# Kernel tuning notes

Measured on AMD Instinct MI355X. Metric: run time of the kernel, lower is better.

The kernel has to match this reference:

```python
import math
import jax, jax.numpy as jnp
import numpy as np

N, CH3, T = 64, 192, 2048

def setup_inputs() -> dict:
    key = jax.random.key(0)
    qkv = jax.random.normal(key, (N, CH3, T), dtype=jnp.float32)
    return {"qkv": qkv}

def reference(qkv):
    ch = qkv.shape[1] // 3
    q, k, v = jnp.split(qkv, 3, axis=1)  # each [b, c, t]
    scale = 1.0 / math.sqrt(math.sqrt(ch))
    # [b, t, s] score matrix (faithful to the naive implementation)
    weight = jnp.einsum('bct,bcs->bts', q * scale, k * scale)
    weight = jax.nn.softmax(weight.astype(jnp.float32), axis=-1).astype(weight.dtype)
    return jnp.einsum('bts,bcs->bct', weight, v)
```

## Files before the change

kernel.cpp:

```cpp
#include <hip/hip_runtime.h>
#include <math.h>


#define B_   64
#define CH_  64
#define T_   2048
#define TQ   128
#define SB   64
#define NIT  (T_ / SB)

typedef __attribute__((ext_vector_type(8))) short short8;
typedef __attribute__((ext_vector_type(4))) float f32x4;
typedef __attribute__((ext_vector_type(4))) unsigned short us4;
typedef __attribute__((ext_vector_type(8))) unsigned short us8;

static __device__ __forceinline__ unsigned short f2bf(float f) {
    union { float f; unsigned u; } v; v.f = f;
    unsigned r = v.u + 0x7FFFu + ((v.u >> 16) & 1u);
    return (unsigned short)(r >> 16);
}

static __device__ __forceinline__ short8 ld_contig(const unsigned short* p) {
    return *(const short8*)p;
}

static __device__ __forceinline__ short8 ld_strided(const unsigned short* p, int stride) {
    short8 r;
#pragma unroll
    for (int j = 0; j < 8; ++j) r[j] = (short)p[j * stride];
    return r;
}

static __device__ __forceinline__ void gl_lds16(const unsigned short* g, unsigned short* l) {
    __builtin_amdgcn_global_load_lds(
        (const __attribute__((address_space(1))) unsigned int*)g,
        (__attribute__((address_space(3))) unsigned int*)l, 16, 0, 0);
}

static __device__ __forceinline__ float vexp2(float x) {
#if __has_builtin(__builtin_amdgcn_exp2f)
    return __builtin_amdgcn_exp2f(x);
#else
    float r;
    asm("v_exp_f32 %0, %1\n\ts_nop 1" : "=v"(r) : "v"(x));
    return r;
#endif
}

static __device__ __forceinline__ unsigned cvtpk(float lo, float hi) {
    unsigned r;
    asm("v_cvt_pk_bf16_f32 %0, %1, %2" : "=v"(r) : "v"(lo), "v"(hi));
    return r;
}

static __device__ __forceinline__ void pl_swap(unsigned& a, unsigned& b) {
    asm volatile("v_permlane32_swap_b32 %0, %1" : "+v"(a), "+v"(b));
    asm volatile("v_permlane16_swap_b32 %0, %1" : "+v"(a), "+v"(b));
}

__global__ __launch_bounds__(256) void qkv_prep(const float* __restrict__ qkv,
                                                unsigned short* __restrict__ Ktg,
                                                unsigned short* __restrict__ Vbg)
{
    __shared__ float Tl[64][65];
    const int tid = threadIdx.x;
    const int b   = blockIdx.x >> 5;
    const int t0  = (blockIdx.x & 31) * 64;
    const float* Kp = qkv + (size_t)b * (3 * CH_ * T_) + (size_t)CH_ * T_;
    const float* Vp = Kp + (size_t)CH_ * T_;

    {
        const int c = tid & 63, fq = tid >> 6;
#pragma unroll
        for (int k = 0; k < 4; ++k) {
            const int tl = 16 * fq + 4 * k;
            const float4 v = *(const float4*)(Kp + (size_t)c * T_ + t0 + tl);
            Tl[c][tl] = v.x; Tl[c][tl + 1] = v.y; Tl[c][tl + 2] = v.z; Tl[c][tl + 3] = v.w;
        }
    }
    {
        const int c = tid >> 2, tq = (tid & 3) * 16;
        unsigned short* vout = Vbg + (size_t)b * CH_ * T_ + (size_t)c * T_ + t0 + tq;
        const float* vin = Vp + (size_t)c * T_ + t0 + tq;
#pragma unroll
        for (int k = 0; k < 2; ++k) {
            const float4 a  = *(const float4*)(vin + 8 * k);
            const float4 bq = *(const float4*)(vin + 8 * k + 4);
            us8 w8;
            w8[0]=f2bf(a.x);  w8[1]=f2bf(a.y);  w8[2]=f2bf(a.z);  w8[3]=f2bf(a.w);
            w8[4]=f2bf(bq.x); w8[5]=f2bf(bq.y); w8[6]=f2bf(bq.z); w8[7]=f2bf(bq.w);
            *(us8*)(vout + 8 * k) = w8;
        }
    }
    __syncthreads();
    {
        const int cb = tid & 7;
#pragma unroll
        for (int ot = 0; ot < 2; ++ot) {
            const int sl = (tid >> 3) + 32 * ot;
            us8 w8;
#pragma unroll
            for (int j = 0; j < 8; ++j) w8[j] = f2bf(Tl[8 * cb + j][sl]);
            *(us8*)(Ktg + (size_t)b * T_ * CH_ + (size_t)(t0 + sl) * 64 + 8 * cb) = w8;
        }
    }
}

__global__ __launch_bounds__(256, 4) void qkv_attn5(const float* __restrict__ qkv,
                                                    const unsigned short* __restrict__ Ktg,
                                                    const unsigned short* __restrict__ Vbg,
                                                    float* __restrict__ out)
{
    __shared__ unsigned short Ks[2][64 * 64];
    __shared__ unsigned short Vs[2][64 * 64];

    const int tid  = threadIdx.x;
    const int lane = tid & 63;
    const int wid  = tid >> 6;
    const int l15  = lane & 15;
    const int h    = lane >> 4;

    int bid = blockIdx.x;
    bid = (bid & 7) * 128 + (bid >> 3);
    const int b  = bid >> 4;
    const int t0 = (bid & 15) * TQ;
    const int tb = t0 + wid * 32;

    const float* Qp = qkv + (size_t)b * (3 * CH_ * T_);
    const unsigned short* Ktb = Ktg + (size_t)b * (T_ * CH_);
    const unsigned short* Vbb = Vbg + (size_t)b * (CH_ * T_);

    const int x0 = 8 * ((h)     ^ (l15 & 7));
    const int x1 = 8 * ((4 + h) ^ (l15 & 7));
    const int rb = l15 * 64;

    const int r0 = tid >> 3;
    const int kx = (tid & 7) ^ (r0 & 7);
    const unsigned short* ksrc0 = Ktb + (size_t)r0 * 64 + 8 * kx;
    const unsigned short* vsrc0 = Vbb + (size_t)r0 * T_ + 8 * kx;

    short8 aq[2][2];
#pragma unroll
    for (int ts = 0; ts < 2; ++ts)
#pragma unroll
        for (int ch = 0; ch < 2; ++ch) {
            short8 q;
#pragma unroll
            for (int j = 0; j < 8; ++j)
                q[j] = (short)f2bf(0.180336880f *
                        Qp[(size_t)(32 * ch + 8 * h + j) * T_ + tb + 16 * ts + l15]);
            aq[ts][ch] = q;
        }

    f32x4 o[4][2];
#pragma unroll
    for (int cs = 0; cs < 4; ++cs)
#pragma unroll
        for (int ts = 0; ts < 2; ++ts) o[cs][ts] = (f32x4){0.f, 0.f, 0.f, 0.f};
    float dsum[2] = {0.f, 0.f};
    const f32x4 zero4 = {0.f, 0.f, 0.f, 0.f};

    gl_lds16(ksrc0,                   &Ks[0][wid * 512]);
    gl_lds16(ksrc0 + 32 * 64,         &Ks[0][wid * 512 + 2048]);
    gl_lds16(vsrc0,                   &Vs[0][wid * 512]);
    gl_lds16(vsrc0 + (size_t)32 * T_, &Vs[0][wid * 512 + 2048]);

    for (int it = 0; it < NIT; ++it) {
        __syncthreads();
        const int buf = it & 1;
        if (it + 1 < NIT) {
            const int s1 = (it + 1) * SB;
            const int bo = (buf ^ 1) * 4096;
            gl_lds16(ksrc0 + (size_t)s1 * 64,        &Ks[0][bo + wid * 512]);
            gl_lds16(ksrc0 + (size_t)(s1 + 32) * 64, &Ks[0][bo + wid * 512 + 2048]);
            gl_lds16(vsrc0 + s1,                     &Vs[0][bo + wid * 512]);
            gl_lds16(vsrc0 + (size_t)32 * T_ + s1,   &Vs[0][bo + wid * 512 + 2048]);
        }
        const unsigned short* kb = &Ks[buf][0];
        const unsigned short* vb = &Vs[buf][0];

        short8 pb[2][2];
#pragma unroll
        for (int half = 0; half < 2; ++half) {
            f32x4 w[2][2];
            __builtin_amdgcn_s_setprio(1);
#pragma unroll
            for (int ss2 = 0; ss2 < 2; ++ss2) {
                const int ss = 2 * half + ss2;
                const short8 bk0 = ld_contig(kb + rb + ss * 1024 + x0);
                const short8 bk1 = ld_contig(kb + rb + ss * 1024 + x1);
#pragma unroll
                for (int ts = 0; ts < 2; ++ts) {
                    f32x4 acc = zero4;
                    acc = __builtin_amdgcn_mfma_f32_16x16x32_bf16(bk0, aq[ts][0], acc, 0, 0, 0);
                    acc = __builtin_amdgcn_mfma_f32_16x16x32_bf16(bk1, aq[ts][1], acc, 0, 0, 0);
                    w[ts][ss2] = acc;
                }
            }
            __builtin_amdgcn_s_setprio(0);
#pragma unroll
            for (int ts = 0; ts < 2; ++ts) {
                float e0[4], e1[4];
#pragma unroll
                for (int r = 0; r < 4; ++r) {
                    e0[r] = vexp2(w[ts][0][r]);
                    e1[r] = vexp2(w[ts][1][r]);
                }
                dsum[ts] += ((e0[0] + e0[1]) + (e0[2] + e0[3]))
                          + ((e1[0] + e1[1]) + (e1[2] + e1[3]));
                unsigned a0 = cvtpk(e0[0], e0[1]);
                unsigned a1 = cvtpk(e0[2], e0[3]);
                unsigned b0 = cvtpk(e1[0], e1[1]);
                unsigned b1 = cvtpk(e1[2], e1[3]);
                pl_swap(a0, b0);
                pl_swap(a1, b1);
                union { short8 s8; unsigned u[4]; } u;
                u.u[0] = a0; u.u[1] = a1; u.u[2] = b0; u.u[3] = b1;
                pb[ts][half] = u.s8;
            }
        }

        __builtin_amdgcn_s_setprio(1);
#pragma unroll
        for (int cs = 0; cs < 4; ++cs) {
            const short8 av0 = ld_contig(vb + rb + cs * 1024 + x0);
            const short8 av1 = ld_contig(vb + rb + cs * 1024 + x1);
#pragma unroll
            for (int ts = 0; ts < 2; ++ts) {
                o[cs][ts] = __builtin_amdgcn_mfma_f32_16x16x32_bf16(av0, pb[ts][0], o[cs][ts], 0, 0, 0);
                o[cs][ts] = __builtin_amdgcn_mfma_f32_16x16x32_bf16(av1, pb[ts][1], o[cs][ts], 0, 0, 0);
            }
        }
        __builtin_amdgcn_s_setprio(0);
    }

    float inv[2];
#pragma unroll
    for (int ts = 0; ts < 2; ++ts) {
        float d = dsum[ts];
        d += __shfl_xor(d, 16, 64);
        d += __shfl_xor(d, 32, 64);
        inv[ts] = 1.0f / d;
    }

    float* outp = out + (size_t)b * CH_ * T_;
#pragma unroll
    for (int cs = 0; cs < 4; ++cs)
#pragma unroll
        for (int r = 0; r < 4; ++r) {
            const size_t row = (size_t)(16 * cs + 4 * h + r) * T_;
            outp[row + tb + l15]      = o[cs][0][r] * inv[0];
            outp[row + tb + 16 + l15] = o[cs][1][r] * inv[1];
        }
}

__global__ __launch_bounds__(256) void qkv_attn_fb(const float* __restrict__ qkv,
                                                   float* __restrict__ out)
{
    __shared__ unsigned short Qs[CH_][68];
    __shared__ unsigned short Ksf[CH_][68];
    __shared__ unsigned short Vsf[CH_][72];
    __shared__ unsigned short Psf[4][64][18];

    const int tid  = threadIdx.x;
    const int lane = tid & 63;
    const int wid  = tid >> 6;
    const int l15  = lane & 15;
    const int h    = lane >> 4;
    const int bidx = blockIdx.x;
    const int b    = bidx >> 5;
    const int t0   = (bidx & 31) * 64;
    const int tw   = wid * 16;

    const float* Qp = qkv + (size_t)b * (3 * CH_ * T_);
    const float* Kp = Qp + CH_ * T_;
    const float* Vp = Kp + CH_ * T_;

    const int srow = tid >> 4;
    const int scol = (tid & 15) << 2;

#pragma unroll
    for (int i = 0; i < 4; ++i) {
        const int c = srow + 16 * i;
        const float4 q = *(const float4*)(Qp + (size_t)c * T_ + t0 + scol);
        us4 w; w[0] = f2bf(q.x); w[1] = f2bf(q.y); w[2] = f2bf(q.z); w[3] = f2bf(q.w);
        *(us4*)(&Qs[c][scol]) = w;
    }
    __syncthreads();

    const short8 aq0 = ld_strided(&Qs[0 + 8 * h][tw + l15], 68);
    const short8 aq1 = ld_strided(&Qs[32 + 8 * h][tw + l15], 68);

    short8 aones;
#pragma unroll
    for (int j = 0; j < 8; ++j) aones[j] = (short)0x3F80;

    f32x4 o[4];
#pragma unroll
    for (int cs = 0; cs < 4; ++cs) o[cs] = (f32x4){0.f, 0.f, 0.f, 0.f};
    float l_run = 0.0f;
    const f32x4 zero4 = {0.f, 0.f, 0.f, 0.f};

    for (int it = 0; it < 32; ++it) {
        const int s0 = it * 64;
        __syncthreads();
#pragma unroll
        for (int i = 0; i < 4; ++i) {
            const int c = srow + 16 * i;
            const float4 kv = *(const float4*)(Kp + (size_t)c * T_ + s0 + scol);
            us4 wk; wk[0] = f2bf(kv.x); wk[1] = f2bf(kv.y); wk[2] = f2bf(kv.z); wk[3] = f2bf(kv.w);
            *(us4*)(&Ksf[c][scol]) = wk;
            const float4 vv = *(const float4*)(Vp + (size_t)c * T_ + s0 + scol);
            us4 wv; wv[0] = f2bf(vv.x); wv[1] = f2bf(vv.y); wv[2] = f2bf(vv.z); wv[3] = f2bf(vv.w);
            *(us4*)(&Vsf[c][scol]) = wv;
        }
        __syncthreads();

        f32x4 w[4];
#pragma unroll
        for (int ss = 0; ss < 4; ++ss) {
            const short8 bkl = ld_strided(&Ksf[0 + 8 * h][ss * 16 + l15], 68);
            const short8 bkh = ld_strided(&Ksf[32 + 8 * h][ss * 16 + l15], 68);
            f32x4 acc = zero4;
            acc = __builtin_amdgcn_mfma_f32_16x16x32_bf16(aq0, bkl, acc, 0, 0, 0);
            acc = __builtin_amdgcn_mfma_f32_16x16x32_bf16(aq1, bkh, acc, 0, 0, 0);
            w[ss] = acc;
        }

#pragma unroll
        for (int ss = 0; ss < 4; ++ss) {
            const float e0 = __expf(0.125f * w[ss][0]);
            const float e1 = __expf(0.125f * w[ss][1]);
            const float e2 = __expf(0.125f * w[ss][2]);
            const float e3 = __expf(0.125f * w[ss][3]);
            const unsigned p01 = (unsigned)f2bf(e0) | ((unsigned)f2bf(e1) << 16);
            const unsigned p23 = (unsigned)f2bf(e2) | ((unsigned)f2bf(e3) << 16);
            const int s = ss * 16 + l15;
            *(unsigned*)(&Psf[wid][s][4 * h]) = p01;
            *(unsigned*)(&Psf[wid][s][4 * h + 2]) = p23;
        }

        const short8 pb0 = ld_strided(&Psf[wid][0 + 8 * h][l15], 18);
        const short8 pb1 = ld_strided(&Psf[wid][32 + 8 * h][l15], 18);

        f32x4 lacc = zero4;
        lacc = __builtin_amdgcn_mfma_f32_16x16x32_bf16(aones, pb0, lacc, 0, 0, 0);
        lacc = __builtin_amdgcn_mfma_f32_16x16x32_bf16(aones, pb1, lacc, 0, 0, 0);
        l_run += lacc[0];

#pragma unroll
        for (int cs = 0; cs < 4; ++cs) {
            const short8 av0 = ld_contig(&Vsf[cs * 16 + l15][0 + 8 * h]);
            const short8 av1 = ld_contig(&Vsf[cs * 16 + l15][32 + 8 * h]);
            o[cs] = __builtin_amdgcn_mfma_f32_16x16x32_bf16(av0, pb0, o[cs], 0, 0, 0);
            o[cs] = __builtin_amdgcn_mfma_f32_16x16x32_bf16(av1, pb1, o[cs], 0, 0, 0);
        }
    }

    const float invd = 1.0f / l_run;
    float* outp = out + (size_t)b * CH_ * T_;
#pragma unroll
    for (int cs = 0; cs < 4; ++cs)
#pragma unroll
        for (int r = 0; r < 4; ++r)
            outp[(size_t)(cs * 16 + 4 * h + r) * T_ + t0 + tw + l15] = o[cs][r] * invd;
}

extern "C" void kernel_launch(void* const* d_in, const int* in_sizes, int n_in,
                              void* d_out, int out_size, void* d_ws, size_t ws_size,
                              hipStream_t stream) {
    const float* qkv = (const float*)d_in[0];
    float* outp = (float*)d_out;
    const size_t need = (size_t)2 * B_ * CH_ * T_ * sizeof(unsigned short);
    if (ws_size >= need) {
        unsigned short* Ktg = (unsigned short*)d_ws;
        unsigned short* Vbg = Ktg + (size_t)B_ * T_ * CH_;
        qkv_prep<<<dim3(B_ * 32), dim3(256), 0, stream>>>(qkv, Ktg, Vbg);
        qkv_attn5<<<dim3(B_ * (T_ / TQ)), dim3(256), 0, stream>>>(qkv, Ktg, Vbg, outp);
    } else {
        qkv_attn_fb<<<dim3(B_ * 32), dim3(256), 0, stream>>>(qkv, outp);
    }
}
```

Measured before the change: 98.10 us.

## Use two waves per block with 64 query columns per wave

After: 101.5 us. 1.03x slower.

```diff
diff --git a/kernel.cpp b/kernel.cpp
--- a/kernel.cpp
+++ b/kernel.cpp
@@ -106,7 +106,7 @@
     }
 }
 
-__global__ __launch_bounds__(256, 4) void qkv_attn5(const float* __restrict__ qkv,
+__global__ __launch_bounds__(128, 2) void qkv_attn6(const float* __restrict__ qkv,
                                                     const unsigned short* __restrict__ Ktg,
                                                     const unsigned short* __restrict__ Vbg,
                                                     float* __restrict__ out)
@@ -124,7 +124,7 @@
     bid = (bid & 7) * 128 + (bid >> 3);
     const int b  = bid >> 4;
     const int t0 = (bid & 15) * TQ;
-    const int tb = t0 + wid * 32;
+    const int tb = t0 + wid * 64;
 
     const float* Qp = qkv + (size_t)b * (3 * CH_ * T_);
     const unsigned short* Ktb = Ktg + (size_t)b * (T_ * CH_);
@@ -138,10 +138,11 @@
     const int kx = (tid & 7) ^ (r0 & 7);
     const unsigned short* ksrc0 = Ktb + (size_t)r0 * 64 + 8 * kx;
     const unsigned short* vsrc0 = Vbb + (size_t)r0 * T_ + 8 * kx;
-
-    short8 aq[2][2];
-#pragma unroll
-    for (int ts = 0; ts < 2; ++ts)
+    const int dbase = 8 * wid * 64;
+
+    short8 aq[4][2];
+#pragma unroll
+    for (int ts = 0; ts < 4; ++ts)
 #pragma unroll
         for (int ch = 0; ch < 2; ++ch) {
             short8 q;
@@ -152,18 +153,19 @@
             aq[ts][ch] = q;
         }
 
-    f32x4 o[4][2];
+    f32x4 o[4][4];
 #pragma unroll
     for (int cs = 0; cs < 4; ++cs)
 #pragma unroll
-        for (int ts = 0; ts < 2; ++ts) o[cs][ts] = (f32x4){0.f, 0.f, 0.f, 0.f};
-    float dsum[2] = {0.f, 0.f};
+        for (int ts = 0; ts < 4; ++ts) o[cs][ts] = (f32x4){0.f, 0.f, 0.f, 0.f};
+    float dsum[4] = {0.f, 0.f, 0.f, 0.f};
     const f32x4 zero4 = {0.f, 0.f, 0.f, 0.f};
 
-    gl_lds16(ksrc0,                   &Ks[0][wid * 512]);
-    gl_lds16(ksrc0 + 32 * 64,         &Ks[0][wid * 512 + 2048]);
-    gl_lds16(vsrc0,                   &Vs[0][wid * 512]);
-    gl_lds16(vsrc0 + (size_t)32 * T_, &Vs[0][wid * 512 + 2048]);
+#pragma unroll
+    for (int j = 0; j < 4; ++j) {
+        gl_lds16(ksrc0 + (size_t)(16 * j) * 64,  &Ks[0][16 * j * 64 + dbase]);
+        gl_lds16(vsrc0 + (size_t)(16 * j) * T_,  &Vs[0][16 * j * 64 + dbase]);
+    }
 
     for (int it = 0; it < NIT; ++it) {
         __syncthreads();
@@ -171,18 +173,21 @@
         if (it + 1 < NIT) {
             const int s1 = (it + 1) * SB;
             const int bo = (buf ^ 1) * 4096;
-            gl_lds16(ksrc0 + (size_t)s1 * 64,        &Ks[0][bo + wid * 512]);
-            gl_lds16(ksrc0 + (size_t)(s1 + 32) * 64, &Ks[0][bo + wid * 512 + 2048]);
-            gl_lds16(vsrc0 + s1,                     &Vs[0][bo + wid * 512]);
-            gl_lds16(vsrc0 + (size_t)32 * T_ + s1,   &Vs[0][bo + wid * 512 + 2048]);
+#pragma unroll
+            for (int j = 0; j < 4; ++j) {
+                gl_lds16(ksrc0 + (size_t)(s1 + 16 * j) * 64,
+                         &Ks[0][bo + 16 * j * 64 + dbase]);
+                gl_lds16(vsrc0 + (size_t)(16 * j) * T_ + s1,
+                         &Vs[0][bo + 16 * j * 64 + dbase]);
+            }
         }
         const unsigned short* kb = &Ks[buf][0];
         const unsigned short* vb = &Vs[buf][0];
 
-        short8 pb[2][2];
+        short8 pb[4][2];
 #pragma unroll
         for (int half = 0; half < 2; ++half) {
-            f32x4 w[2][2];
+            f32x4 w[4][2];
             __builtin_amdgcn_s_setprio(1);
 #pragma unroll
             for (int ss2 = 0; ss2 < 2; ++ss2) {
@@ -190,7 +195,7 @@
                 const short8 bk0 = ld_contig(kb + rb + ss * 1024 + x0);
                 const short8 bk1 = ld_contig(kb + rb + ss * 1024 + x1);
 #pragma unroll
-                for (int ts = 0; ts < 2; ++ts) {
+                for (int ts = 0; ts < 4; ++ts) {
                     f32x4 acc = zero4;
                     acc = __builtin_amdgcn_mfma_f32_16x16x32_bf16(bk0, aq[ts][0], acc, 0, 0, 0);
                     acc = __builtin_amdgcn_mfma_f32_16x16x32_bf16(bk1, aq[ts][1], acc, 0, 0, 0);
@@ -199,7 +204,7 @@
             }
             __builtin_amdgcn_s_setprio(0);
 #pragma unroll
-            for (int ts = 0; ts < 2; ++ts) {
+            for (int ts = 0; ts < 4; ++ts) {
                 float e0[4], e1[4];
 #pragma unroll
                 for (int r = 0; r < 4; ++r) {
@@ -226,7 +231,7 @@
             const short8 av0 = ld_contig(vb + rb + cs * 1024 + x0);
             const short8 av1 = ld_contig(vb + rb + cs * 1024 + x1);
 #pragma unroll
-            for (int ts = 0; ts < 2; ++ts) {
+            for (int ts = 0; ts < 4; ++ts) {
                 o[cs][ts] = __builtin_amdgcn_mfma_f32_16x16x32_bf16(av0, pb[ts][0], o[cs][ts], 0, 0, 0);
                 o[cs][ts] = __builtin_amdgcn_mfma_f32_16x16x32_bf16(av1, pb[ts][1], o[cs][ts], 0, 0, 0);
             }
@@ -234,9 +239,9 @@
         __builtin_amdgcn_s_setprio(0);
     }
 
-    float inv[2];
-#pragma unroll
-    for (int ts = 0; ts < 2; ++ts) {
+    float inv[4];
+#pragma unroll
+    for (int ts = 0; ts < 4; ++ts) {
         float d = dsum[ts];
         d += __shfl_xor(d, 16, 64);
         d += __shfl_xor(d, 32, 64);
@@ -249,8 +254,9 @@
 #pragma unroll
         for (int r = 0; r < 4; ++r) {
             const size_t row = (size_t)(16 * cs + 4 * h + r) * T_;
-            outp[row + tb + l15]      = o[cs][0][r] * inv[0];
-            outp[row + tb + 16 + l15] = o[cs][1][r] * inv[1];
+#pragma unroll
+            for (int ts = 0; ts < 4; ++ts)
+                outp[row + tb + 16 * ts + l15] = o[cs][ts][r] * inv[ts];
         }
 }
 
@@ -376,7 +382,7 @@
         unsigned short* Ktg = (unsigned short*)d_ws;
         unsigned short* Vbg = Ktg + (size_t)B_ * T_ * CH_;
         qkv_prep<<<dim3(B_ * 32), dim3(256), 0, stream>>>(qkv, Ktg, Vbg);
-        qkv_attn5<<<dim3(B_ * (T_ / TQ)), dim3(256), 0, stream>>>(qkv, Ktg, Vbg, outp);
+        qkv_attn6<<<dim3(B_ * (T_ / TQ)), dim3(128), 0, stream>>>(qkv, Ktg, Vbg, outp);
     } else {
         qkv_attn_fb<<<dim3(B_ * 32), dim3(256), 0, stream>>>(qkv, outp);
     }
```
